# Kernel optimization log

Measured on AMD Instinct MI355X. Metric: run time of the kernel, lower is better.

The kernel has to match this reference:

```python
import jax, jax.numpy as jnp
import numpy as np

MAX_SET_SIZE = 8


def setup_inputs() -> dict:
    key = jax.random.key(0)
    ks = jax.random.split(key, 8)
    n_items, L, d_v = 8192, 64, 128
    n_chains, hidden = 32768, 128
    v = jax.random.normal(ks[0], (n_items, L, d_v), dtype=jnp.float32)
    batch_idx = jax.random.randint(ks[1], (n_chains,), 0, n_items, dtype=jnp.int32)
    mask = jax.random.randint(ks[2], (n_chains, L), 0, 2) > 0
    count = jax.random.randint(ks[3], (n_chains,), 0, 64, dtype=jnp.int32)
    in_dim = MAX_SET_SIZE * d_v + 1
    W1 = jax.random.normal(ks[4], (in_dim, hidden), dtype=jnp.float32) / np.sqrt(in_dim)
    b1 = jnp.zeros((hidden,), dtype=jnp.float32)
    W2 = jax.random.normal(ks[5], (hidden, d_v), dtype=jnp.float32) / np.sqrt(hidden)
    b2 = jnp.zeros((d_v,), dtype=jnp.float32)
    return {"v": v, "batch_idx": batch_idx, "mask": mask, "count": count,
            "W1": W1, "b1": b1, "W2": W2, "b2": b2}


def reference(v, batch_idx, mask, count, W1, b1, W2, b2):
    n_chains, L = mask.shape
    d_v = v.shape[-1]
    K = MAX_SET_SIZE  # k_keep = min(max_set_size, L) = 8 since L >= 8
    # score = mask * (L - pos): earlier positions score higher; top_k picks
    # the first K masked positions (ties impossible among masked entries).
    pos = jnp.arange(L, dtype=jnp.float32)
    scores = mask.astype(jnp.float32) * (jnp.float32(L) - pos)[None, :]
    top_scores, top_idx = jax.lax.top_k(scores, K)        # [n_chains, K]
    picked = top_scores > 0
    sortable = jnp.where(picked, top_idx, L)              # sentinel L for unpicked
    order = jnp.argsort(sortable, axis=1)                 # restore index order
    sortable = jnp.take_along_axis(sortable, order, axis=1)
    picked = jnp.take_along_axis(picked, order, axis=1)
    safe_idx = jnp.where(picked, sortable, 0)
    # Fused gather: v[batch_idx[c], safe_idx[c, k], :] -> [n_chains, K, d_v]
    packed = v[batch_idx[:, None], safe_idx]
    packed = packed * picked[..., None].astype(v.dtype)
    flat = packed.reshape(n_chains, K * d_v)
    log_count = jnp.log1p(count.astype(v.dtype))[:, None]
    x = jnp.concatenate([flat, log_count], axis=-1)       # [n_chains, K*d_v + 1]
    h = jax.nn.gelu(x @ W1 + b1, approximate=False)       # exact GELU (torch default)
    return h @ W2 + b2
```

## Files before the change

kernel.cpp:

```cpp
#include <hip/hip_runtime.h>
#include <hip/hip_bf16.h>
#include <math.h>


typedef __attribute__((ext_vector_type(8))) short bf16x8;
typedef __attribute__((ext_vector_type(4))) float f32x4;

#define NCHAINS 32768
#define LPOS    64
#define DV      128
#define HID     128
#define KDIM    1024
#define CPB     32

__device__ __forceinline__ unsigned short cvt_bf16(float a) {
  unsigned u = __float_as_uint(a);
  u += 0x7fffu + ((u >> 16) & 1u);
  return (unsigned short)(u >> 16);
}
__device__ __forceinline__ unsigned pk2_bf16(float a, float b) {
  unsigned ua = __float_as_uint(a), ub = __float_as_uint(b);
  ua += 0x7fffu + ((ua >> 16) & 1u);
  ub += 0x7fffu + ((ub >> 16) & 1u);
  return (ua >> 16) | (ub & 0xffff0000u);
}
__device__ __forceinline__ float gelu_exact(float x) {
  return 0.5f * x * (1.0f + erff(x * 0.70710678118654752f));
}

__global__ __launch_bounds__(256) void prep_kernel(
    const float* __restrict__ W1, const float* __restrict__ W2,
    unsigned short* __restrict__ W1p, unsigned short* __restrict__ W2p,
    float* __restrict__ zr) {
  int id = blockIdx.x * 256 + threadIdx.x;
  {
    int j = id & 7, lx = (id >> 3) & 63, nt = (id >> 9) & 7, ch = id >> 12;
    int k = ch * 32 + ((lx >> 4) & 3) * 8 + j;
    int n = nt * 16 + (lx & 15);
    W1p[id] = cvt_bf16(W1[k * HID + n]);
    if (id < 16384) {
      int ch2 = id >> 12;
      int k2 = ch2 * 32 + ((lx >> 4) & 3) * 8 + j;
      W2p[id] = cvt_bf16(W2[k2 * HID + n]);
    }
  }
  if (id < DV) zr[id] = 0.0f;
}

__global__ __launch_bounds__(256, 8) void gather_pack_kernel(
    const float* __restrict__ v, const int* __restrict__ batch_idx,
    const int* __restrict__ mask,
    const float* __restrict__ zr, unsigned short* __restrict__ Xp) {
  __shared__ const float* s_rp[16][8];

  const int tid = threadIdx.x;
  const int ht = blockIdx.x;

  if (tid < 16) {
    int c = ht * 16 + tid;
    const int4* mp = (const int4*)(mask + (size_t)c * LPOS);
    unsigned long long m64 = 0;
    #pragma unroll
    for (int q = 0; q < 16; q++) {
      int4 mm = mp[q];
      unsigned long long b = (mm.x != 0 ? 1ull : 0ull) | (mm.y != 0 ? 2ull : 0ull) |
                             (mm.z != 0 ? 4ull : 0ull) | (mm.w != 0 ? 8ull : 0ull);
      m64 |= b << (q * 4);
    }
    const float* base = v + (size_t)batch_idx[c] * (LPOS * DV);
    #pragma unroll
    for (int s = 0; s < 8; s++) {
      const float* p;
      if (m64) {
        int pos = __ffsll(m64) - 1;
        m64 &= (m64 - 1);
        p = base + pos * DV;
      } else {
        p = zr;
      }
      s_rp[tid][s] = p;
    }
  }
  __syncthreads();

  const int w = tid >> 6, l = tid & 63;
  const int m = l >> 2, kq = l & 3;
  const int g = w * 64 + ((l >> 2) | ((l & 3) << 4));
  const int koff = w * 32 + kq * 8;

  const float* p[8];
  #pragma unroll
  for (int s = 0; s < 8; s++) p[s] = s_rp[m][s];

  uint4* dst = (uint4*)(Xp + (size_t)ht * 16384) + g;

  #pragma unroll
  for (int i = 0; i < 8; i++) {
    const float* src = p[i] + koff;
    float4 x0 = *(const float4*)src;
    float4 x1 = *(const float4*)(src + 4);
    uint4 o;
    o.x = pk2_bf16(x0.x, x0.y);
    o.y = pk2_bf16(x0.z, x0.w);
    o.z = pk2_bf16(x1.x, x1.y);
    o.w = pk2_bf16(x1.z, x1.w);
    dst[i * 256] = o;
  }
}

__global__ __launch_bounds__(256, 4) void gemm_kernel(
    const int* __restrict__ count,
    const float* __restrict__ W1, const float* __restrict__ b1,
    const float* __restrict__ b2,
    const unsigned short* __restrict__ W1p, const unsigned short* __restrict__ W2p,
    const unsigned short* __restrict__ Xp, float* __restrict__ out) {
  __shared__ float s_logc[CPB];
  __shared__ unsigned short s_H[CPB][HID + 8];

  const int tid = threadIdx.x;
  const int blk = blockIdx.x;

  if (tid < CPB) s_logc[tid] = log1pf((float)count[blk * CPB + tid]);
  __syncthreads();

  const int l = tid & 63, w = tid >> 6;
  const int mh = w & 1, cb = w >> 1;
  const int m = l & 15, kq = l >> 4;

  const unsigned short* ap = Xp + (size_t)(2 * blk + mh) * 16384 + l * 8;
  const unsigned short* bp = W1p + ((size_t)(cb * 4) * 64 + l) * 8;

  f32x4 acc0 = {0.f,0.f,0.f,0.f}, acc1 = {0.f,0.f,0.f,0.f};
  f32x4 acc2 = {0.f,0.f,0.f,0.f}, acc3 = {0.f,0.f,0.f,0.f};

  #pragma unroll 2
  for (int ch = 0; ch < 32; ch++) {
    bf16x8 a = *(const bf16x8*)(ap + (size_t)ch * 512);
    const unsigned short* wb = bp + (size_t)ch * 4096;
    bf16x8 b0 = *(const bf16x8*)(wb);
    bf16x8 b1f = *(const bf16x8*)(wb + 512);
    bf16x8 b2f = *(const bf16x8*)(wb + 1024);
    bf16x8 b3f = *(const bf16x8*)(wb + 1536);
    acc0 = __builtin_amdgcn_mfma_f32_16x16x32_bf16(a, b0,  acc0, 0, 0, 0);
    acc1 = __builtin_amdgcn_mfma_f32_16x16x32_bf16(a, b1f, acc1, 0, 0, 0);
    acc2 = __builtin_amdgcn_mfma_f32_16x16x32_bf16(a, b2f, acc2, 0, 0, 0);
    acc3 = __builtin_amdgcn_mfma_f32_16x16x32_bf16(a, b3f, acc3, 0, 0, 0);
  }

  {
    float w1l[4], b1v[4];
    #pragma unroll
    for (int nt = 0; nt < 4; nt++) {
      int n = cb * 64 + nt * 16 + m;
      w1l[nt] = W1[KDIM * HID + n];
      b1v[nt] = b1[n];
    }
    f32x4* accs[4] = {&acc0, &acc1, &acc2, &acc3};
    #pragma unroll
    for (int r = 0; r < 4; r++) {
      int row = mh * 16 + kq * 4 + r;
      float lc = s_logc[row];
      #pragma unroll
      for (int nt = 0; nt < 4; nt++) {
        float h = (*accs[nt])[r] + lc * w1l[nt] + b1v[nt];
        s_H[row][cb * 64 + nt * 16 + m] = cvt_bf16(gelu_exact(h));
      }
    }
  }
  __syncthreads();

  f32x4 d0 = {0.f,0.f,0.f,0.f}, d1 = {0.f,0.f,0.f,0.f};
  f32x4 d2 = {0.f,0.f,0.f,0.f}, d3 = {0.f,0.f,0.f,0.f};

  #pragma unroll
  for (int ch = 0; ch < 4; ch++) {
    bf16x8 a = *(const bf16x8*)&s_H[mh * 16 + m][ch * 32 + kq * 8];
    const unsigned short* wb = W2p + ((size_t)(ch * 8 + cb * 4) * 64 + l) * 8;
    bf16x8 b0 = *(const bf16x8*)(wb);
    bf16x8 b1f = *(const bf16x8*)(wb + 512);
    bf16x8 b2f = *(const bf16x8*)(wb + 1024);
    bf16x8 b3f = *(const bf16x8*)(wb + 1536);
    d0 = __builtin_amdgcn_mfma_f32_16x16x32_bf16(a, b0,  d0, 0, 0, 0);
    d1 = __builtin_amdgcn_mfma_f32_16x16x32_bf16(a, b1f, d1, 0, 0, 0);
    d2 = __builtin_amdgcn_mfma_f32_16x16x32_bf16(a, b2f, d2, 0, 0, 0);
    d3 = __builtin_amdgcn_mfma_f32_16x16x32_bf16(a, b3f, d3, 0, 0, 0);
  }

  {
    float b2v[4];
    #pragma unroll
    for (int nt = 0; nt < 4; nt++) b2v[nt] = b2[cb * 64 + nt * 16 + m];
    f32x4* ds[4] = {&d0, &d1, &d2, &d3};
    #pragma unroll
    for (int r = 0; r < 4; r++) {
      int row = mh * 16 + kq * 4 + r;
      size_t o = (size_t)(blk * CPB + row) * DV;
      #pragma unroll
      for (int nt = 0; nt < 4; nt++) {
        out[o + cb * 64 + nt * 16 + m] = (*ds[nt])[r] + b2v[nt];
      }
    }
  }
}

extern "C" void kernel_launch(void* const* d_in, const int* in_sizes, int n_in,
                              void* d_out, int out_size, void* d_ws, size_t ws_size,
                              hipStream_t stream) {
  const float* v          = (const float*)d_in[0];
  const int* batch_idx    = (const int*)d_in[1];
  const int* mk           = (const int*)d_in[2];
  const int* count        = (const int*)d_in[3];
  const float* W1         = (const float*)d_in[4];
  const float* b1         = (const float*)d_in[5];
  const float* W2         = (const float*)d_in[6];
  const float* b2         = (const float*)d_in[7];
  float* out              = (float*)d_out;

  char* ws = (char*)d_ws;
  unsigned short* W1p = (unsigned short*)ws;
  unsigned short* W2p = (unsigned short*)(ws + 262144);
  float* zr           = (float*)(ws + 262144 + 32768);
  unsigned short* Xp  = (unsigned short*)(ws + 262144 + 32768 + 512);

  prep_kernel<<<512, 256, 0, stream>>>(W1, W2, W1p, W2p, zr);
  gather_pack_kernel<<<NCHAINS / 16, 256, 0, stream>>>(v, batch_idx, mk, zr, Xp);
  gemm_kernel<<<NCHAINS / CPB, 256, 0, stream>>>(
      count, W1, b1, b2, W1p, W2p, Xp, out);
}
```

Measured before the change: 373.3 us.

## Fuse gather-pack into GEMM kernel, converting gathered rows to bf16 in registers

Merges the gather/pack kernel into the MLP GEMM kernel. Each block now resolves row pointers for its 32 chains and loads the fp32 v rows straight into MFMA A-operand registers, converting to bf16 on the fly. This removes the Xp intermediate write and re-read (about 64 MB of traffic) and one kernel launch. In exchange, gather latency is no longer overlapped by a separate high-occupancy kernel and must be hidden inside the GEMM loop, at lower occupancy and with each row read by several waves.

```diff
diff --git a/kernel.cpp b/kernel.cpp
--- a/kernel.cpp
+++ b/kernel.cpp
@@ -5,6 +5,7 @@
 
 typedef __attribute__((ext_vector_type(8))) short bf16x8;
 typedef __attribute__((ext_vector_type(4))) float f32x4;
+typedef __attribute__((ext_vector_type(4))) unsigned int u32x4;
 
 #define NCHAINS 32768
 #define LPOS    64
@@ -47,17 +48,23 @@
   if (id < DV) zr[id] = 0.0f;
 }
 
-__global__ __launch_bounds__(256, 8) void gather_pack_kernel(
+__global__ __launch_bounds__(256, 4) void fused_kernel(
     const float* __restrict__ v, const int* __restrict__ batch_idx,
-    const int* __restrict__ mask,
-    const float* __restrict__ zr, unsigned short* __restrict__ Xp) {
-  __shared__ const float* s_rp[16][8];
+    const int* __restrict__ mask, const int* __restrict__ count,
+    const float* __restrict__ W1, const float* __restrict__ b1,
+    const float* __restrict__ b2,
+    const unsigned short* __restrict__ W1p, const unsigned short* __restrict__ W2p,
+    const float* __restrict__ zr, float* __restrict__ out) {
+  __shared__ const float* s_rp[CPB][9];
+  __shared__ float s_logc[CPB];
+  __shared__ unsigned short s_H[CPB][HID + 8];
 
   const int tid = threadIdx.x;
-  const int ht = blockIdx.x;
-
-  if (tid < 16) {
-    int c = ht * 16 + tid;
+  const int blk = blockIdx.x;
+
+  if (tid < CPB) {
+    int c = blk * CPB + tid;
+    s_logc[tid] = log1pf((float)count[c]);
     const int4* mp = (const int4*)(mask + (size_t)c * LPOS);
     unsigned long long m64 = 0;
     #pragma unroll
@@ -83,68 +90,40 @@
   }
   __syncthreads();
 
-  const int w = tid >> 6, l = tid & 63;
-  const int m = l >> 2, kq = l & 3;
-  const int g = w * 64 + ((l >> 2) | ((l & 3) << 4));
-  const int koff = w * 32 + kq * 8;
-
-  const float* p[8];
-  #pragma unroll
-  for (int s = 0; s < 8; s++) p[s] = s_rp[m][s];
-
-  uint4* dst = (uint4*)(Xp + (size_t)ht * 16384) + g;
-
-  #pragma unroll
-  for (int i = 0; i < 8; i++) {
-    const float* src = p[i] + koff;
-    float4 x0 = *(const float4*)src;
-    float4 x1 = *(const float4*)(src + 4);
-    uint4 o;
-    o.x = pk2_bf16(x0.x, x0.y);
-    o.y = pk2_bf16(x0.z, x0.w);
-    o.z = pk2_bf16(x1.x, x1.y);
-    o.w = pk2_bf16(x1.z, x1.w);
-    dst[i * 256] = o;
-  }
-}
-
-__global__ __launch_bounds__(256, 4) void gemm_kernel(
-    const int* __restrict__ count,
-    const float* __restrict__ W1, const float* __restrict__ b1,
-    const float* __restrict__ b2,
-    const unsigned short* __restrict__ W1p, const unsigned short* __restrict__ W2p,
-    const unsigned short* __restrict__ Xp, float* __restrict__ out) {
-  __shared__ float s_logc[CPB];
-  __shared__ unsigned short s_H[CPB][HID + 8];
-
-  const int tid = threadIdx.x;
-  const int blk = blockIdx.x;
-
-  if (tid < CPB) s_logc[tid] = log1pf((float)count[blk * CPB + tid]);
-  __syncthreads();
-
   const int l = tid & 63, w = tid >> 6;
   const int mh = w & 1, cb = w >> 1;
   const int m = l & 15, kq = l >> 4;
-
-  const unsigned short* ap = Xp + (size_t)(2 * blk + mh) * 16384 + l * 8;
+  const int mrow = mh * 16 + m;
+
   const unsigned short* bp = W1p + ((size_t)(cb * 4) * 64 + l) * 8;
 
   f32x4 acc0 = {0.f,0.f,0.f,0.f}, acc1 = {0.f,0.f,0.f,0.f};
   f32x4 acc2 = {0.f,0.f,0.f,0.f}, acc3 = {0.f,0.f,0.f,0.f};
 
-  #pragma unroll 2
-  for (int ch = 0; ch < 32; ch++) {
-    bf16x8 a = *(const bf16x8*)(ap + (size_t)ch * 512);
-    const unsigned short* wb = bp + (size_t)ch * 4096;
-    bf16x8 b0 = *(const bf16x8*)(wb);
-    bf16x8 b1f = *(const bf16x8*)(wb + 512);
-    bf16x8 b2f = *(const bf16x8*)(wb + 1024);
-    bf16x8 b3f = *(const bf16x8*)(wb + 1536);
-    acc0 = __builtin_amdgcn_mfma_f32_16x16x32_bf16(a, b0,  acc0, 0, 0, 0);
-    acc1 = __builtin_amdgcn_mfma_f32_16x16x32_bf16(a, b1f, acc1, 0, 0, 0);
-    acc2 = __builtin_amdgcn_mfma_f32_16x16x32_bf16(a, b2f, acc2, 0, 0, 0);
-    acc3 = __builtin_amdgcn_mfma_f32_16x16x32_bf16(a, b3f, acc3, 0, 0, 0);
+  #pragma unroll
+  for (int s = 0; s < 8; s++) {
+    const float* ps = s_rp[mrow][s] + kq * 8;
+    #pragma unroll
+    for (int dc = 0; dc < 4; dc++) {
+      const int ch = s * 4 + dc;
+      float4 x0 = *(const float4*)(ps + dc * 32);
+      float4 x1 = *(const float4*)(ps + dc * 32 + 4);
+      u32x4 ua;
+      ua.x = pk2_bf16(x0.x, x0.y);
+      ua.y = pk2_bf16(x0.z, x0.w);
+      ua.z = pk2_bf16(x1.x, x1.y);
+      ua.w = pk2_bf16(x1.z, x1.w);
+      bf16x8 a = __builtin_bit_cast(bf16x8, ua);
+      const unsigned short* wb = bp + (size_t)ch * 4096;
+      bf16x8 b0  = *(const bf16x8*)(wb);
+      bf16x8 b1f = *(const bf16x8*)(wb + 512);
+      bf16x8 b2f = *(const bf16x8*)(wb + 1024);
+      bf16x8 b3f = *(const bf16x8*)(wb + 1536);
+      acc0 = __builtin_amdgcn_mfma_f32_16x16x32_bf16(a, b0,  acc0, 0, 0, 0);
+      acc1 = __builtin_amdgcn_mfma_f32_16x16x32_bf16(a, b1f, acc1, 0, 0, 0);
+      acc2 = __builtin_amdgcn_mfma_f32_16x16x32_bf16(a, b2f, acc2, 0, 0, 0);
+      acc3 = __builtin_amdgcn_mfma_f32_16x16x32_bf16(a, b3f, acc3, 0, 0, 0);
+    }
   }
 
   {
@@ -176,7 +155,7 @@
   for (int ch = 0; ch < 4; ch++) {
     bf16x8 a = *(const bf16x8*)&s_H[mh * 16 + m][ch * 32 + kq * 8];
     const unsigned short* wb = W2p + ((size_t)(ch * 8 + cb * 4) * 64 + l) * 8;
-    bf16x8 b0 = *(const bf16x8*)(wb);
+    bf16x8 b0  = *(const bf16x8*)(wb);
     bf16x8 b1f = *(const bf16x8*)(wb + 512);
     bf16x8 b2f = *(const bf16x8*)(wb + 1024);
     bf16x8 b3f = *(const bf16x8*)(wb + 1536);
@@ -220,10 +199,8 @@
   unsigned short* W1p = (unsigned short*)ws;
   unsigned short* W2p = (unsigned short*)(ws + 262144);
   float* zr           = (float*)(ws + 262144 + 32768);
-  unsigned short* Xp  = (unsigned short*)(ws + 262144 + 32768 + 512);
 
   prep_kernel<<<512, 256, 0, stream>>>(W1, W2, W1p, W2p, zr);
-  gather_pack_kernel<<<NCHAINS / 16, 256, 0, stream>>>(v, batch_idx, mk, zr, Xp);
-  gemm_kernel<<<NCHAINS / CPB, 256, 0, stream>>>(
-      count, W1, b1, b2, W1p, W2p, Xp, out);
-}
+  fused_kernel<<<NCHAINS / CPB, 256, 0, stream>>>(
+      v, batch_idx, mk, count, W1, b1, b2, W1p, W2p, zr, out);
+}
```

Result: no change. 377.9 us (+1.2%).
